# Optimization experiments

Measured on AMD Instinct MI355X. Metric: run time of the kernel, lower is better.

## Reference

```python
import jax, jax.numpy as jnp
import numpy as np

N = 100000          # nodes
E = 3200000         # edges (avg degree 32)
NODE_IN = 128
H = 64              # hidden_feats
B = 2048            # graphs in batch
MP_STEPS = 3
S2S_STEPS = 3
D = 3 * H           # Set2Set in_channels = 192
READOUT = 1024


def setup_inputs() -> dict:
    key = jax.random.key(0)
    ks = jax.random.split(key, 32)
    p = lambda k, shape: (jax.random.normal(k, shape, dtype=jnp.float32) * 0.05)
    inp = {
        "x": jax.random.normal(ks[0], (N, NODE_IN), dtype=jnp.float32),
        "edge_index": jax.random.randint(ks[1], (2, E), 0, N, dtype=jnp.int64),
        "edge_attr": jax.random.normal(ks[2], (E, 16), dtype=jnp.float32),
        "batch": jnp.sort(jax.random.randint(ks[3], (N,), 0, B, dtype=jnp.int64)),
        # project_node_feats
        "W_p": p(ks[4], (H, NODE_IN)), "b_p": p(ks[5], (H,)),
        # SAGEConv: lin_l (on mean-aggregated neighbors, with bias) + lin_r (root, no bias)
        "W_l": p(ks[6], (H, H)), "b_l": p(ks[7], (H,)), "W_r": p(ks[8], (H, H)),
        # gate nets (Linear(H,1)+Sigmoid)
        "gs_W": p(ks[9], (1, H)), "gs_b": p(ks[10], (1,)),
        "gr_W": p(ks[11], (1, H)), "gr_b": p(ks[12], (1,)),
        # GRU_s / GRU_r (single layer, gate order r,z,n as in torch)
        "grus_Wih": p(ks[13], (3 * H, H)), "grus_Whh": p(ks[14], (3 * H, H)),
        "grus_bih": p(ks[15], (3 * H,)), "grus_bhh": p(ks[16], (3 * H,)),
        "grur_Wih": p(ks[17], (3 * H, H)), "grur_Whh": p(ks[18], (3 * H, H)),
        "grur_bih": p(ks[19], (3 * H,)), "grur_bhh": p(ks[20], (3 * H,)),
        # Set2Set LSTM: input 2D -> hidden D (gate order i,f,g,o)
        "lstm_Wih": p(ks[21], (4 * D, 2 * D)), "lstm_Whh": p(ks[22], (4 * D, D)),
        "lstm_bih": p(ks[23], (4 * D,)), "lstm_bhh": p(ks[24], (4 * D,)),
        # sparsify: Linear(2D=6H, readout) + PReLU(scalar, init 0.25)
        "W_sp": p(ks[25], (READOUT, 2 * D)), "b_sp": p(ks[26], (READOUT,)),
        "prelu_a": jnp.float32(0.25),
    }
    return inp


def _gru_cell(x, h, Wih, Whh, bih, bhh):
    gi = x @ Wih.T + bih
    gh = h @ Whh.T + bhh
    ir, iz, inn = jnp.split(gi, 3, axis=-1)
    hr, hz, hn = jnp.split(gh, 3, axis=-1)
    r = jax.nn.sigmoid(ir + hr)
    z = jax.nn.sigmoid(iz + hz)
    n = jnp.tanh(inn + r * hn)
    return (1.0 - z) * n + z * h


def _lstm_cell(x, h, c, Wih, Whh, bih, bhh):
    g = x @ Wih.T + bih + h @ Whh.T + bhh
    i, f, gg, o = jnp.split(g, 4, axis=-1)
    c_new = jax.nn.sigmoid(f) * c + jax.nn.sigmoid(i) * jnp.tanh(gg)
    h_new = jax.nn.sigmoid(o) * jnp.tanh(c_new)
    return h_new, c_new


def reference(x, edge_index, edge_attr, batch,
              W_p, b_p, W_l, b_l, W_r, gs_W, gs_b, gr_W, gr_b,
              grus_Wih, grus_Whh, grus_bih, grus_bhh,
              grur_Wih, grur_Whh, grur_bih, grur_bhh,
              lstm_Wih, lstm_Whh, lstm_bih, lstm_bhh,
              W_sp, b_sp, prelu_a):
    src, dst = edge_index[0], edge_index[1]
    deg = jnp.maximum(jax.ops.segment_sum(jnp.ones((E,), x.dtype), dst, num_segments=N), 1.0)

    proj = jax.nn.relu(x @ W_p.T + b_p)                     # [N, H]
    h_s = proj
    h_r = proj
    gates_r = []
    for _ in range(MP_STEPS):
        # SAGEConv(mean): lin_l(mean_j x_j) + lin_r(x_i)
        agg = jax.ops.segment_sum(h_s[src], dst, num_segments=N) / deg[:, None]
        m = agg @ W_l.T + b_l + h_s @ W_r.T
        am = jax.nn.relu(m)
        gate_s = jax.nn.sigmoid(h_s @ gs_W.T + gs_b)        # [N, 1]
        h_s_new = _gru_cell(gate_s * am, h_s, grus_Wih, grus_Whh, grus_bih, grus_bhh)
        gate_r = jax.nn.sigmoid(h_r @ gr_W.T + gr_b)        # [N, 1]
        gates_r.append(gate_r)
        h_r = _gru_cell(gate_r * am, h_r, grur_Wih, grur_Whh, grur_bih, grur_bhh)
        h_s = h_s_new

    feats = jnp.concatenate([proj, h_s, h_r], axis=1)       # [N, 3H=D]

    # Set2Set readout over ragged graph segments
    q_star = jnp.zeros((B, 2 * D), feats.dtype)
    hl = jnp.zeros((B, D), feats.dtype)
    cl = jnp.zeros((B, D), feats.dtype)
    for _ in range(S2S_STEPS):
        hl, cl = _lstm_cell(q_star, hl, cl, lstm_Wih, lstm_Whh, lstm_bih, lstm_bhh)
        q = hl                                              # [B, D]
        e = jnp.sum(feats * q[batch], axis=-1)              # [N]
        mmax = jax.ops.segment_max(e, batch, num_segments=B)
        ex = jnp.exp(e - mmax[batch])
        denom = jax.ops.segment_sum(ex, batch, num_segments=B)
        a = ex / denom[batch]                               # segment softmax
        r = jax.ops.segment_sum(a[:, None] * feats, batch, num_segments=B)  # [B, D]
        q_star = jnp.concatenate([q, r], axis=1)            # [B, 2D]

    z = q_star @ W_sp.T + b_sp                              # [B, READOUT]
    graph_feats = jnp.where(z >= 0, z, prelu_a * z)         # PReLU
    return graph_feats, jnp.stack(gates_r)                  # [B,1024], [MP_STEPS,N,1]
```

## Files before the change

kernel.cpp:

```cpp
#include <hip/hip_runtime.h>
#include <math.h>

#define NN 100000
#define NE 3200000
#define NIN 128
#define HH 64
#define NB 2048
#define RO 1024

#define NT    1563
#define NBK   391
#define BINB  782
#define GCB   391
#define PCAP  10240
#define PREPN 63488
#define PREPB 248

typedef unsigned short u16;
typedef __attribute__((ext_vector_type(8))) short short8;
typedef __attribute__((ext_vector_type(4))) float f32x4;

__device__ __forceinline__ float sigmoidf_(float x){ return 1.f/(1.f+expf(-x)); }
__device__ __forceinline__ float dot4_(float4 a, float4 b){ return a.x*b.x + a.y*b.y + a.z*b.z + a.w*b.w; }
__device__ __forceinline__ u16 f2bf(float f){
  unsigned u = __float_as_uint(f);
  return (u16)((u + 0x7FFFu + ((u>>16)&1u)) >> 16);
}
__device__ __forceinline__ float bf2f(u16 v){
  return __uint_as_float(((unsigned)v) << 16);
}

__global__ void k_bkcnt_prep(const int* __restrict__ dst, const int* __restrict__ batch,
                             int* __restrict__ bkcnt, int* __restrict__ gcnt,
                             const float* __restrict__ Wp, const float* __restrict__ Wl,
                             const float* __restrict__ Wr,
                             const float* __restrict__ sWih, const float* __restrict__ sWhh,
                             const float* __restrict__ rWih, const float* __restrict__ rWhh,
                             const float* __restrict__ lWih, const float* __restrict__ lWhh,
                             u16* __restrict__ pB_proj, u16* __restrict__ pB_sage,
                             u16* __restrict__ pB_gruS, u16* __restrict__ pB_gruR,
                             u16* __restrict__ pB_lstm){
  __shared__ int hist[NBK];
  const int t = threadIdx.x;
  if (blockIdx.x < BINB){
    for (int i = t; i < NBK; i += 256) hist[i] = 0;
    __syncthreads();
    const int e0 = blockIdx.x * 4096;
    const int cntE = min(4096, NE - e0);
    for (int idx = t; idx < cntE; idx += 256)
      atomicAdd(&hist[dst[e0 + idx] >> 8], 1);
    __syncthreads();
    for (int i = t; i < NBK; i += 256)
      if (hist[i]) atomicAdd(&bkcnt[i], hist[i]);
    return;
  }
  int r = blockIdx.x - BINB;
  if (r < GCB){
    int n = r*256 + t;
    if (n < NN) atomicAdd(&gcnt[batch[n]], 1);
    return;
  }
  int id = (r - GCB)*256 + t;
  if (id >= PREPN) return;
  const float* sp; u16* d;
  if (id < 1024){
    int fi = id; d = pB_proj + (size_t)fi*8;
    int lane = fi&63, kt=(fi>>6)&3, ct=fi>>8;
    int rr = ct*16 + (lane&15), k0 = kt*32 + (lane>>4)*8;
    sp = &Wp[(size_t)rr*NIN + k0];
  } else if (id < 2048){
    int fi = id - 1024; d = pB_sage + (size_t)fi*8;
    int lane = fi&63, kt=(fi>>6)&3, ct=fi>>8;
    int rr = ct*16 + (lane&15), k0 = kt*32 + (lane>>4)*8;
    sp = (k0 < 64) ? &Wl[(size_t)rr*HH + k0] : &Wr[(size_t)rr*HH + (k0-64)];
  } else if (id < 8192){
    int base = id - 2048;
    const float* Wih; const float* Whh; u16* pb; int fi;
    if (base < 3072){ pb = pB_gruS; Wih = sWih; Whh = sWhh; fi = base; }
    else            { pb = pB_gruR; Wih = rWih; Whh = rWhh; fi = base - 3072; }
    int lane = fi&63, kt=(fi>>6)&1, c2=fi>>7;
    const float* W2 = (c2 < 12) ? Wih : Whh;
    int ct = (c2 < 12) ? c2 : c2 - 12;
    int rr = ct*16 + (lane&15), k0 = kt*32 + (lane>>4)*8;
    sp = &W2[(size_t)rr*HH + k0];
    d = pb + (size_t)fi*8;
  } else {
    int fi = id - 8192;
    int ctg = fi / 1152;
    int rem = fi - ctg*1152;
    int ktg = rem >> 6, lane = rem & 63;
    int rr = ctg*16 + (lane&15), k0 = ktg*32 + (lane>>4)*8;
    sp = (k0 < 384) ? &lWih[(size_t)rr*384 + k0] : &lWhh[(size_t)rr*192 + (k0-384)];
    d = pB_lstm + (size_t)fi*8;
  }
  #pragma unroll
  for (int q = 0; q < 8; ++q) d[q] = f2bf(sp[q]);
}

__global__ __launch_bounds__(256) void k_scan_small(
    const int* __restrict__ bkcnt, int* __restrict__ bkbase, int* __restrict__ bcur,
    const int* __restrict__ gcnt, int* __restrict__ growptr){
  __shared__ int sb[256];
  const int t = threadIdx.x;
  if (blockIdx.x == 0){
    int loc[2]; int s = 0;
    #pragma unroll
    for (int q = 0; q < 2; ++q){ int i = t*2+q; loc[q] = (i < NBK) ? bkcnt[i] : 0; s += loc[q]; }
    sb[t] = s; __syncthreads();
    int v = s;
    for (int o = 1; o < 256; o <<= 1){
      int u = (t >= o) ? sb[t-o] : 0; __syncthreads();
      sb[t] += u; __syncthreads();
    }
    int run = sb[t] - v;
    #pragma unroll
    for (int q = 0; q < 2; ++q){
      int i = t*2+q;
      if (i < NBK){ bkbase[i] = run; bcur[i] = run; run += loc[q]; }
    }
    if (t == 255) bkbase[NBK] = run;
  } else {
    int base = t*8;
    int loc[8]; int s = 0;
    #pragma unroll
    for (int q = 0; q < 8; ++q){ loc[q] = gcnt[base+q]; s += loc[q]; }
    sb[t] = s; __syncthreads();
    int v = s;
    for (int o = 1; o < 256; o <<= 1){
      int u = (t >= o) ? sb[t-o] : 0; __syncthreads();
      sb[t] += u; __syncthreads();
    }
    int run = sb[t] - v;
    #pragma unroll
    for (int q = 0; q < 8; ++q){ growptr[base+q] = run; run += loc[q]; }
    if (t == 255) growptr[NB] = run;
  }
}

__global__ __launch_bounds__(256) void k_bin(
    const int* __restrict__ src, const int* __restrict__ dst,
    int* __restrict__ bcur, int2* __restrict__ binned)
{
  __shared__ int hist[NBK];
  __shared__ int lbase[NBK];
  __shared__ int gbase[NBK];
  __shared__ int sb[512];
  __shared__ int2 stage[4096];
  const int t = threadIdx.x;
  const int e0 = blockIdx.x * 4096;
  const int cntE = min(4096, NE - e0);
  for (int i = t; i < NBK; i += 256) hist[i] = 0;
  __syncthreads();
  int2 ed[16];
  #pragma unroll
  for (int k = 0; k < 16; ++k){
    int idx = (k<<8) + t;
    if (idx < cntE){
      int e = e0 + idx;
      ed[k].x = src[e]; ed[k].y = dst[e];
      atomicAdd(&hist[ed[k].y >> 8], 1);
    } else ed[k].y = -1;
  }
  __syncthreads();
  sb[t]     = (t < NBK) ? hist[t] : 0;
  sb[t+256] = (t+256 < NBK) ? hist[t+256] : 0;
  __syncthreads();
  for (int off = 1; off < 512; off <<= 1){
    int v0 = (t >= off)     ? sb[t-off]     : 0;
    int v1 = (t+256 >= off) ? sb[t+256-off] : 0;
    __syncthreads();
    sb[t] += v0; sb[t+256] += v1;
    __syncthreads();
  }
  if (t < NBK)     lbase[t]     = sb[t]     - hist[t];
  if (t+256 < NBK) lbase[t+256] = sb[t+256] - hist[t+256];
  if (t < NBK)     gbase[t]     = (hist[t]     > 0) ? atomicAdd(&bcur[t],     hist[t])     : 0;
  if (t+256 < NBK) gbase[t+256] = (hist[t+256] > 0) ? atomicAdd(&bcur[t+256], hist[t+256]) : 0;
  __syncthreads();
  for (int i = t; i < NBK; i += 256) hist[i] = 0;
  __syncthreads();
  #pragma unroll
  for (int k = 0; k < 16; ++k){
    if (ed[k].y >= 0){
      int b = ed[k].y >> 8;
      int r = atomicAdd(&hist[b], 1);
      stage[lbase[b] + r] = ed[k];
    }
  }
  __syncthreads();
  for (int i = t; i < cntE; i += 256){
    int2 e = stage[i];
    int b = e.y >> 8;
    binned[gbase[b] + (i - lbase[b])] = e;
  }
}

__global__ __launch_bounds__(256) void k_place(
    const int2* __restrict__ binned, const int* __restrict__ bkbase,
    int* __restrict__ rowptr, int* __restrict__ col)
{
  __shared__ int h[256];
  __shared__ int cur[256];
  __shared__ int sb2[256];
  __shared__ int stage[PCAP];
  const int t = threadIdx.x;
  const int b = blockIdx.x;
  const int n0 = b << 8;
  const int B0 = bkbase[b], B1 = bkbase[b+1];
  const int cntE = B1 - B0;
  h[t] = 0; __syncthreads();
  for (int i = t; i < cntE; i += 256){
    int2 e = binned[B0 + i];
    atomicAdd(&h[e.y - n0], 1);
  }
  __syncthreads();
  sb2[t] = h[t]; __syncthreads();
  for (int off = 1; off < 256; off <<= 1){
    int v = (t >= off) ? sb2[t-off] : 0;
    __syncthreads();
    sb2[t] += v;
    __syncthreads();
  }
  int pre = sb2[t] - h[t];
  if (n0 + t < NN) rowptr[n0 + t] = B0 + pre;
  if (b == NBK-1 && t == 0) rowptr[NN] = B1;
  if (cntE <= PCAP){
    cur[t] = pre;
    __syncthreads();
    for (int i = t; i < cntE; i += 256){
      int2 e = binned[B0 + i];
      int idx = atomicAdd(&cur[e.y - n0], 1);
      stage[idx] = e.x;
    }
    __syncthreads();
    for (int i = t; i < cntE; i += 256) col[B0 + i] = stage[i];
  } else {
    cur[t] = B0 + pre;
    __syncthreads();
    for (int i = t; i < cntE; i += 256){
      int2 e = binned[B0 + i];
      int p = atomicAdd(&cur[e.y - n0], 1);
      col[p] = e.x;
    }
  }
}

__global__ __launch_bounds__(256) void k_proj(
    const float* __restrict__ x, const u16* __restrict__ pB, const float* __restrict__ bp,
    float* __restrict__ proj, float* __restrict__ hs, float* __restrict__ hr,
    u16* __restrict__ hsb)
{
  __shared__ u16 s_a[64][136];
  __shared__ u16 s_b[4*4*64*8];
  __shared__ float s_bias[64];
  const int t = threadIdx.x;
  const int n0 = blockIdx.x * 64;
  for (int idx = t; idx < 1024; idx += 256)
    ((short8*)s_b)[idx] = ((const short8*)pB)[idx];
  if (t < 64) s_bias[t] = bp[t];
  {
    int r = t>>2, cg = t&3, node = n0 + r;
    u16* d = &s_a[r][cg*32];
    if (node < NN){
      const float4* xp = (const float4*)&x[(size_t)node*NIN + cg*32];
      #pragma unroll
      for (int q = 0; q < 8; ++q){
        float4 v = xp[q];
        d[q*4+0]=f2bf(v.x); d[q*4+1]=f2bf(v.y); d[q*4+2]=f2bf(v.z); d[q*4+3]=f2bf(v.w);
      }
    } else {
      #pragma unroll
      for (int q = 0; q < 32; ++q) d[q] = 0;
    }
  }
  __syncthreads();
  const int lane = t & 63, nt = t >> 6;
  const int colp = lane & 15, rowg = lane >> 4;
  f32x4 acc[4];
  #pragma unroll
  for (int i = 0; i < 4; ++i) acc[i] = (f32x4){0.f,0.f,0.f,0.f};
  #pragma unroll
  for (int kt = 0; kt < 4; ++kt){
    short8 a = *(const short8*)&s_a[nt*16 + colp][kt*32 + rowg*8];
    #pragma unroll
    for (int ct = 0; ct < 4; ++ct){
      short8 b = *(const short8*)&s_b[((ct*4 + kt)*64 + lane)*8];
      acc[ct] = __builtin_amdgcn_mfma_f32_16x16x32_bf16(a, b, acc[ct], 0, 0, 0);
    }
  }
  #pragma unroll
  for (int reg = 0; reg < 4; ++reg){
    int node = n0 + nt*16 + rowg*4 + reg;
    if (node >= NN) continue;
    #pragma unroll
    for (int ct = 0; ct < 4; ++ct){
      int j = ct*16 + colp;
      float v = fmaxf(acc[ct][reg] + s_bias[j], 0.f);
      size_t o = (size_t)node*HH + j;
      proj[o] = v; hs[o] = v; hr[o] = v;
      hsb[o] = f2bf(v);
    }
  }
}

__global__ __launch_bounds__(256) void k_agg(
    const u16* __restrict__ hb, const int* __restrict__ rowptr,
    const int* __restrict__ col, u16* __restrict__ aggb)
{
  int node = blockIdx.x*4 + (threadIdx.x >> 6);
  int lane = threadIdx.x & 63;
  if (node >= NN) return;
  int beg = rowptr[node], end = rowptr[node+1];
  const int slot = lane >> 3;
  const int c8 = (lane & 7) * 8;
  float a0=0.f,a1=0.f,a2=0.f,a3=0.f,a4=0.f,a5=0.f,a6=0.f,a7=0.f;
  for (int i = beg + slot; i < end; i += 8){
    int nb = col[i];
    short8 v = *(const short8*)&hb[(size_t)nb*HH + c8];
    a0 += bf2f((u16)v[0]); a1 += bf2f((u16)v[1]);
    a2 += bf2f((u16)v[2]); a3 += bf2f((u16)v[3]);
    a4 += bf2f((u16)v[4]); a5 += bf2f((u16)v[5]);
    a6 += bf2f((u16)v[6]); a7 += bf2f((u16)v[7]);
  }
  #pragma unroll
  for (int m = 8; m <= 32; m <<= 1){
    a0 += __shfl_xor(a0, m); a1 += __shfl_xor(a1, m);
    a2 += __shfl_xor(a2, m); a3 += __shfl_xor(a3, m);
    a4 += __shfl_xor(a4, m); a5 += __shfl_xor(a5, m);
    a6 += __shfl_xor(a6, m); a7 += __shfl_xor(a7, m);
  }
  if (slot == 0){
    float invd = 1.f / fmaxf((float)(end - beg), 1.f);
    short8 o;
    o[0]=(short)f2bf(a0*invd); o[1]=(short)f2bf(a1*invd);
    o[2]=(short)f2bf(a2*invd); o[3]=(short)f2bf(a3*invd);
    o[4]=(short)f2bf(a4*invd); o[5]=(short)f2bf(a5*invd);
    o[6]=(short)f2bf(a6*invd); o[7]=(short)f2bf(a7*invd);
    *(short8*)&aggb[(size_t)node*HH + c8] = o;
  }
}

__global__ __launch_bounds__(256) void k_sage(
    const u16* __restrict__ hsb, const u16* __restrict__ pB,
    const float* __restrict__ bl, u16* __restrict__ aggb)
{
  __shared__ u16 s_a[64][136];
  __shared__ u16 s_b[4*4*64*8];
  __shared__ float s_bias[64];
  const int t = threadIdx.x;
  const int n0 = blockIdx.x * 64;
  for (int idx = t; idx < 1024; idx += 256)
    ((short8*)s_b)[idx] = ((const short8*)pB)[idx];
  if (t < 64) s_bias[t] = bl[t];
  {
    int r = t>>2, cg = t&3, node = n0 + r;
    short8* d8 = (short8*)&s_a[r][cg*32];
    if (node < NN){
      const short8* sp = (cg < 2) ? (const short8*)&aggb[(size_t)node*HH + cg*32]
                                  : (const short8*)&hsb[(size_t)node*HH + (cg-2)*32];
      d8[0] = sp[0]; d8[1] = sp[1]; d8[2] = sp[2]; d8[3] = sp[3];
    } else {
      u16* dz = (u16*)d8;
      #pragma unroll
      for (int q = 0; q < 32; ++q) dz[q] = 0;
    }
  }
  __syncthreads();
  const int lane = t & 63, nt = t >> 6;
  const int colp = lane & 15, rowg = lane >> 4;
  f32x4 acc[4];
  #pragma unroll
  for (int i = 0; i < 4; ++i) acc[i] = (f32x4){0.f,0.f,0.f,0.f};
  #pragma unroll
  for (int kt = 0; kt < 4; ++kt){
    short8 a = *(const short8*)&s_a[nt*16 + colp][kt*32 + rowg*8];
    #pragma unroll
    for (int ct = 0; ct < 4; ++ct){
      short8 b = *(const short8*)&s_b[((ct*4 + kt)*64 + lane)*8];
      acc[ct] = __builtin_amdgcn_mfma_f32_16x16x32_bf16(a, b, acc[ct], 0, 0, 0);
    }
  }
  __syncthreads();
  #pragma unroll
  for (int reg = 0; reg < 4; ++reg){
    int node = n0 + nt*16 + rowg*4 + reg;
    if (node >= NN) continue;
    #pragma unroll
    for (int ct = 0; ct < 4; ++ct){
      int j = ct*16 + colp;
      float v = fmaxf(acc[ct][reg] + s_bias[j], 0.f);
      aggb[(size_t)node*HH + j] = f2bf(v);
    }
  }
}

__global__ __launch_bounds__(256) void k_gru(
    float* __restrict__ h, const u16* __restrict__ amb,
    const float* __restrict__ gW, const float* __restrict__ gb,
    const u16* __restrict__ pB,
    const float* __restrict__ bih, const float* __restrict__ bhh,
    float* __restrict__ out_gate, u16* __restrict__ bfout)
{
  __shared__ u16 s_b[2*12*2*64*8];
  __shared__ u16 s_x[64][72];
  __shared__ u16 s_h[64][72];
  __shared__ float s_bi[192], s_bh[192];
  const int t = threadIdx.x;
  const int n0 = blockIdx.x * 64;
  for (int idx = t; idx < 3072; idx += 256)
    ((short8*)s_b)[idx] = ((const short8*)pB)[idx];
  if (t < 192){ s_bi[t] = bih[t]; s_bh[t] = bhh[t]; }
  const float gb0 = gb[0];
  {
    int r = t>>2, cg = t&3, node = n0 + r;
    u16* dh = &s_h[r][cg*16];
    u16* dx = &s_x[r][cg*16];
    if (node < NN){
      float hv[16];
      const float4* hp = (const float4*)&h[(size_t)node*HH + cg*16];
      #pragma unroll
      for (int q = 0; q < 4; ++q){
        float4 v = hp[q];
        hv[q*4+0]=v.x; hv[q*4+1]=v.y; hv[q*4+2]=v.z; hv[q*4+3]=v.w;
      }
      const float* gwp = &gW[cg*16];
      float p = 0.f;
      #pragma unroll
      for (int q = 0; q < 16; ++q) p += hv[q]*gwp[q];
      p += __shfl_xor(p, 1);
      p += __shfl_xor(p, 2);
      float gate = sigmoidf_(p + gb0);
      if (out_gate != nullptr && cg == 0) out_gate[node] = gate;
      #pragma unroll
      for (int q = 0; q < 16; ++q) dh[q] = f2bf(hv[q]);
      const short8* ap = (const short8*)&amb[(size_t)node*HH + cg*16];
      short8 a0 = ap[0], a1 = ap[1];
      #pragma unroll
      for (int q = 0; q < 8; ++q){
        dx[q]   = f2bf(gate * bf2f((u16)a0[q]));
        dx[8+q] = f2bf(gate * bf2f((u16)a1[q]));
      }
    } else {
      #pragma unroll
      for (int q = 0; q < 16; ++q){ dh[q] = 0; dx[q] = 0; }
    }
  }
  __syncthreads();
  const int lane = t & 63, nt = t >> 6;
  const int colp = lane & 15, rowg = lane >> 4;
  f32x4 acc[24];
  #pragma unroll
  for (int i = 0; i < 24; ++i) acc[i] = (f32x4){0.f,0.f,0.f,0.f};
  const int arow = nt*16 + colp;
  #pragma unroll
  for (int kt = 0; kt < 2; ++kt){
    short8 ax = *(const short8*)&s_x[arow][kt*32 + rowg*8];
    short8 ah = *(const short8*)&s_h[arow][kt*32 + rowg*8];
    #pragma unroll
    for (int ct = 0; ct < 12; ++ct){
      short8 b0 = *(const short8*)&s_b[((ct*2 + kt)*64 + lane)*8];
      acc[ct] = __builtin_amdgcn_mfma_f32_16x16x32_bf16(ax, b0, acc[ct], 0, 0, 0);
      short8 b1 = *(const short8*)&s_b[(((12 + ct)*2 + kt)*64 + lane)*8];
      acc[12+ct] = __builtin_amdgcn_mfma_f32_16x16x32_bf16(ah, b1, acc[12+ct], 0, 0, 0);
    }
  }
  #pragma unroll
  for (int reg = 0; reg < 4; ++reg){
    int node = n0 + nt*16 + rowg*4 + reg;
    if (node >= NN) continue;
    #pragma unroll
    for (int jt = 0; jt < 4; ++jt){
      int j = jt*16 + colp;
      float ir = acc[jt][reg]      + s_bi[j];
      float iz = acc[4+jt][reg]    + s_bi[64+j];
      float in_ = acc[8+jt][reg]   + s_bi[128+j];
      float hr_ = acc[12+jt][reg]  + s_bh[j];
      float hz = acc[16+jt][reg]   + s_bh[64+j];
      float hn = acc[20+jt][reg]   + s_bh[128+j];
      float rg = sigmoidf_(ir + hr_);
      float zg = sigmoidf_(iz + hz);
      float ng = tanhf(in_ + rg*hn);
      size_t o = (size_t)node*HH + j;
      float ho = h[o];
      float hv = (1.f - zg)*ng + zg*ho;
      h[o] = hv;
      if (bfout != nullptr) bfout[o] = f2bf(hv);
    }
  }
}

__global__ __launch_bounds__(256) void k_lstmg(
    const float* __restrict__ q_star, const float* __restrict__ hin,
    const u16* __restrict__ pBl, const float* __restrict__ bih, const float* __restrict__ bhh,
    float* __restrict__ gbuf)
{
  __shared__ u16 s_a[64][72];
  __shared__ u16 s_b[6*2*64*8];
  const int t = threadIdx.x;
  const int mt = blockIdx.x >> 3, ntile = blockIdx.x & 7;
  const int g0 = mt * 64, c0 = ntile * 96;
  const int lane = t & 63, nt = t >> 6;
  const int colp = lane & 15, rowg = lane >> 4;
  f32x4 acc[6];
  #pragma unroll
  for (int ct = 0; ct < 6; ++ct){
    int j = c0 + ct*16 + colp;
    float bb = bih[j] + bhh[j];
    acc[ct] = (f32x4){bb, bb, bb, bb};
  }
  const int r = t>>2, cg = t&3;
  for (int kc = 0; kc < 9; ++kc){
    {
      const float* srcp = (kc < 6) ? &q_star[(size_t)(g0+r)*384 + kc*64 + cg*16]
                                   : &hin[(size_t)(g0+r)*192 + (kc-6)*64 + cg*16];
      u16* d = &s_a[r][cg*16];
      const float4* xp = (const float4*)srcp;
      #pragma unroll
      for (int q = 0; q < 4; ++q){
        float4 v = xp[q];
        d[q*4+0]=f2bf(v.x); d[q*4+1]=f2bf(v.y); d[q*4+2]=f2bf(v.z); d[q*4+3]=f2bf(v.w);
      }
    }
    for (int idx2 = t; idx2 < 768; idx2 += 256){
      int ctl = idx2 >> 7, rem = idx2 & 127;
      int ktl = rem >> 6, lane2 = rem & 63;
      int fsrc = ((ntile*6 + ctl)*18 + (kc*2 + ktl))*64 + lane2;
      ((short8*)s_b)[(ctl*2 + ktl)*64 + lane2] = ((const short8*)pBl)[fsrc];
    }
    __syncthreads();
    const int arow = nt*16 + colp;
    #pragma unroll
    for (int ktl = 0; ktl < 2; ++ktl){
      short8 a = *(const short8*)&s_a[arow][ktl*32 + rowg*8];
      #pragma unroll
      for (int ct = 0; ct < 6; ++ct){
        short8 b = *(const short8*)&s_b[((ct*2 + ktl)*64 + lane)*8];
        acc[ct] = __builtin_amdgcn_mfma_f32_16x16x32_bf16(a, b, acc[ct], 0, 0, 0);
      }
    }
    __syncthreads();
  }
  #pragma unroll
  for (int reg = 0; reg < 4; ++reg){
    int g = g0 + nt*16 + rowg*4 + reg;
    #pragma unroll
    for (int ct = 0; ct < 6; ++ct){
      int j = c0 + ct*16 + colp;
      gbuf[(size_t)g*768 + j] = acc[ct][reg];
    }
  }
}

__global__ __launch_bounds__(192) void k_lstm_ep(
    const float* __restrict__ gbuf, const float* __restrict__ cin,
    float* __restrict__ hout, float* __restrict__ cout)
{
  const int g = blockIdx.x, d = threadIdx.x;
  const float* gp = &gbuf[(size_t)g*768];
  float i_ = gp[d], f_ = gp[192+d], gg = gp[384+d], o_ = gp[576+d];
  float c = sigmoidf_(f_)*cin[(size_t)g*192 + d] + sigmoidf_(i_)*tanhf(gg);
  float hn = sigmoidf_(o_)*tanhf(c);
  cout[(size_t)g*192 + d] = c;
  hout[(size_t)g*192 + d] = hn;
}

__global__ __launch_bounds__(256) void k_attn2(
    const float* __restrict__ proj, const float* __restrict__ hs, const float* __restrict__ hr,
    const float* __restrict__ hl, const int* __restrict__ growptr,
    float* __restrict__ q_star)
{
  __shared__ float s_q[192];
  __shared__ float s_e[512];
  __shared__ float red[256];
  const int b = blockIdx.x;
  const int beg = growptr[b], end = growptr[b+1];
  const int cnt = end - beg;
  const int t = threadIdx.x, wv = t>>6, lane = t&63;
  if (t < 192) s_q[t] = hl[(size_t)b*192 + t];
  __syncthreads();
  const float q0 = s_q[lane], q1 = s_q[64+lane], q2 = s_q[128+lane];
  const float* fbase = (t < 64) ? proj : (t < 128) ? hs : hr;
  const int fcol = lane;
  float m_run = -3.0e38f, d_run = 0.f, racc = 0.f;
  for (int c0 = 0; c0 < cnt; c0 += 512){
    int cc = min(512, cnt - c0);
    for (int i = wv; i < cc; i += 4){
      size_t o = (size_t)(beg + c0 + i)*HH;
      float v = proj[o+lane]*q0 + hs[o+lane]*q1 + hr[o+lane]*q2;
      #pragma unroll
      for (int off = 32; off > 0; off >>= 1) v += __shfl_down(v, off);
      if (lane == 0) s_e[i] = v;
    }
    __syncthreads();
    float mx = -3.0e38f;
    for (int i = t; i < cc; i += 256) mx = fmaxf(mx, s_e[i]);
    red[t] = mx; __syncthreads();
    for (int s = 128; s > 0; s >>= 1){ if (t < s) red[t] = fmaxf(red[t], red[t+s]); __syncthreads(); }
    float nm = fmaxf(m_run, red[0]);
    __syncthreads();
    float ps = 0.f;
    for (int i = t; i < cc; i += 256){ float ex = expf(s_e[i] - nm); s_e[i] = ex; ps += ex; }
    red[t] = ps; __syncthreads();
    for (int s = 128; s > 0; s >>= 1){ if (t < s) red[t] += red[t+s]; __syncthreads(); }
    float scale = (m_run > -1.0e38f) ? expf(m_run - nm) : 0.f;
    d_run = d_run*scale + red[0];
    racc *= scale;
    if (t < 192){
      for (int i = 0; i < cc; ++i)
        racc += s_e[i] * fbase[(size_t)(beg + c0 + i)*HH + fcol];
    }
    m_run = nm;
    __syncthreads();
  }
  if (t < 192){
    q_star[(size_t)b*384 + t] = s_q[t];
    q_star[(size_t)b*384 + 192 + t] = (cnt > 0) ? racc/d_run : 0.f;
  }
}

__global__ __launch_bounds__(256) void k_final(
    const float* __restrict__ q_star, const float* __restrict__ W, const float* __restrict__ bias,
    const float* __restrict__ prelu_a, float* __restrict__ out)
{
  __shared__ float s_q[8][384];
  const int t = threadIdx.x;
  const int b0 = blockIdx.x * 8;
  for (int i = t; i < 8*384; i += 256){ int g=i/384, k=i%384; s_q[g][k] = q_star[(size_t)(b0+g)*384 + k]; }
  __syncthreads();
  float a = prelu_a[0];
  float acc[4][8];
  #pragma unroll
  for (int m = 0; m < 4; ++m){
    float bb = bias[t + 256*m];
    #pragma unroll
    for (int g = 0; g < 8; ++g) acc[m][g] = bb;
  }
  for (int k4 = 0; k4 < 96; ++k4){
    float4 w0 = *(const float4*)&W[(size_t)(t)*384     + k4*4];
    float4 w1 = *(const float4*)&W[(size_t)(t+256)*384 + k4*4];
    float4 w2 = *(const float4*)&W[(size_t)(t+512)*384 + k4*4];
    float4 w3 = *(const float4*)&W[(size_t)(t+768)*384 + k4*4];
    #pragma unroll
    for (int g = 0; g < 8; ++g){
      float4 q = *(const float4*)&s_q[g][k4*4];
      acc[0][g] += dot4_(w0,q); acc[1][g] += dot4_(w1,q);
      acc[2][g] += dot4_(w2,q); acc[3][g] += dot4_(w3,q);
    }
  }
  #pragma unroll
  for (int m = 0; m < 4; ++m){
    int j = t + 256*m;
    #pragma unroll
    for (int g = 0; g < 8; ++g){
      float z = acc[m][g];
      out[(size_t)(b0+g)*RO + j] = (z >= 0.f) ? z : a*z;
    }
  }
}

extern "C" void kernel_launch(void* const* d_in, const int* in_sizes, int n_in,
                              void* d_out, int out_size, void* d_ws, size_t ws_size,
                              hipStream_t stream) {
  const float* x       = (const float*)d_in[0];
  const int*   ei      = (const int*)d_in[1];
  const int*   batch   = (const int*)d_in[3];
  const float* W_p     = (const float*)d_in[4];
  const float* b_p     = (const float*)d_in[5];
  const float* W_l     = (const float*)d_in[6];
  const float* b_l     = (const float*)d_in[7];
  const float* W_r     = (const float*)d_in[8];
  const float* gs_W    = (const float*)d_in[9];
  const float* gs_b    = (const float*)d_in[10];
  const float* gr_W    = (const float*)d_in[11];
  const float* gr_b    = (const float*)d_in[12];
  const float* grus_Wih= (const float*)d_in[13];
  const float* grus_Whh= (const float*)d_in[14];
  const float* grus_bih= (const float*)d_in[15];
  const float* grus_bhh= (const float*)d_in[16];
  const float* grur_Wih= (const float*)d_in[17];
  const float* grur_Whh= (const float*)d_in[18];
  const float* grur_bih= (const float*)d_in[19];
  const float* grur_bhh= (const float*)d_in[20];
  const float* lstm_Wih= (const float*)d_in[21];
  const float* lstm_Whh= (const float*)d_in[22];
  const float* lstm_bih= (const float*)d_in[23];
  const float* lstm_bhh= (const float*)d_in[24];
  const float* W_sp    = (const float*)d_in[25];
  const float* b_sp    = (const float*)d_in[26];
  const float* prelu_a = (const float*)d_in[27];

  float* out = (float*)d_out;
  char* w = (char*)d_ws;
  size_t off = 0;
  auto A = [&](size_t bytes){ size_t o = off; off += (bytes + 255) & ~(size_t)255; return o; };

  int*   bkcnt   = (int*)(w + A((size_t)NBK*4));
  int*   bkbase  = (int*)(w + A((size_t)(NBK+1)*4));
  int*   bcur    = (int*)(w + A((size_t)NBK*4));
  int*   rowptr  = (int*)(w + A((size_t)(NN+1)*4));
  int*   col     = (int*)(w + A((size_t)NE*4));
  int2*  binned  = (int2*)(w + A((size_t)NE*8));
  int*   gcnt    = (int*)(w + A((size_t)NB*4));
  int*   growptr = (int*)(w + A((size_t)(NB+1)*4));
  float* proj    = (float*)(w + A((size_t)NN*HH*4));
  float* hs      = (float*)(w + A((size_t)NN*HH*4));
  float* hr      = (float*)(w + A((size_t)NN*HH*4));
  u16*   hsb     = (u16*)(w + A((size_t)NN*HH*2));
  u16*   aggb    = (u16*)(w + A((size_t)NN*HH*2));
  float* qstar   = (float*)(w + A((size_t)NB*384*4));
  float* hlA     = (float*)(w + A((size_t)NB*192*4));
  float* clA     = (float*)(w + A((size_t)NB*192*4));
  float* hlB     = (float*)(w + A((size_t)NB*192*4));
  float* clB     = (float*)(w + A((size_t)NB*192*4));
  float* gbuf    = (float*)(w + A((size_t)NB*768*4));
  u16*   pB_proj = (u16*)(w + A((size_t)8192*2));
  u16*   pB_sage = (u16*)(w + A((size_t)8192*2));
  u16*   pB_gruS = (u16*)(w + A((size_t)24576*2));
  u16*   pB_gruR = (u16*)(w + A((size_t)24576*2));
  u16*   pB_lstm = (u16*)(w + A((size_t)55296*8*2));

  const int* src = ei;
  const int* dst = ei + NE;

  hipMemsetAsync(bkcnt, 0, (size_t)NBK*4, stream);
  hipMemsetAsync(gcnt,  0, (size_t)NB*4, stream);
  hipMemsetAsync(qstar, 0, (size_t)NB*384*4, stream);
  hipMemsetAsync(hlA,   0, (size_t)NB*192*4, stream);
  hipMemsetAsync(clA,   0, (size_t)NB*192*4, stream);

  k_bkcnt_prep<<<BINB + GCB + PREPB, 256, 0, stream>>>(dst, batch, bkcnt, gcnt,
                                                       W_p, W_l, W_r, grus_Wih, grus_Whh,
                                                       grur_Wih, grur_Whh, lstm_Wih, lstm_Whh,
                                                       pB_proj, pB_sage, pB_gruS, pB_gruR, pB_lstm);
  k_scan_small<<<2, 256, 0, stream>>>(bkcnt, bkbase, bcur, gcnt, growptr);
  k_bin  <<<BINB, 256, 0, stream>>>(src, dst, bcur, binned);
  k_place<<<NBK, 256, 0, stream>>>(binned, bkbase, rowptr, col);
  k_proj <<<NT, 256, 0, stream>>>(x, pB_proj, b_p, proj, hs, hr, hsb);

  float* gates_out = out + (size_t)NB*RO;
  for (int s = 0; s < 3; ++s){
    k_agg <<<NN/4, 256, 0, stream>>>(hsb, rowptr, col, aggb);
    k_sage<<<NT, 256, 0, stream>>>(hsb, pB_sage, b_l, aggb);
    k_gru <<<NT, 256, 0, stream>>>(hs, aggb, gs_W, gs_b, pB_gruS,
                                   grus_bih, grus_bhh, (float*)nullptr, hsb);
    k_gru <<<NT, 256, 0, stream>>>(hr, aggb, gr_W, gr_b, pB_gruR,
                                   grur_bih, grur_bhh, gates_out + (size_t)s*NN, (u16*)nullptr);
  }

  float* hin = hlA; float* cin = clA; float* hout = hlB; float* cout_ = clB;
  for (int t = 0; t < 3; ++t){
    k_lstmg  <<<256, 256, 0, stream>>>(qstar, hin, pB_lstm, lstm_bih, lstm_bhh, gbuf);
    k_lstm_ep<<<NB, 192, 0, stream>>>(gbuf, cin, hout, cout_);
    k_attn2  <<<NB, 256, 0, stream>>>(proj, hs, hr, hout, growptr, qstar);
    float* th = hin; hin = hout; hout = th;
    float* tc = cin; cin = cout_; cout_ = tc;
  }

  k_final<<<NB/8, 256, 0, stream>>>(qstar, W_sp, b_sp, prelu_a, out);
}
```

Baseline: 843.3 us.

## Pack binned edges, merge GRU launches, fuse LSTM epilogue, use bf16 feats and MFMA readout

Edges are binned as a single packed int (17-bit src plus 8-bit local dst), which halves binned traffic in k_bin and k_place. The two GRU kernels per step are merged into one launch with twice the blocks. The LSTM epilogue is fused into the attention kernel. Set2Set attention now reads bf16 copies of proj/hs/hr instead of fp32. The final readout linear becomes a bf16 MFMA GEMM with pre-packed weights. The bf16 reads and bf16 GEMM lower precision, and the packing assumes src fits in 17 bits (N=100000 does).

```diff
diff --git a/kernel.cpp b/kernel.cpp
--- a/kernel.cpp
+++ b/kernel.cpp
@@ -13,15 +13,15 @@
 #define BINB  782
 #define GCB   391
 #define PCAP  10240
-#define PREPN 63488
-#define PREPB 248
+#define PREPN 112640
+#define PREPB 440
+#define SRCMASK 0x1FFFF
 
 typedef unsigned short u16;
 typedef __attribute__((ext_vector_type(8))) short short8;
 typedef __attribute__((ext_vector_type(4))) float f32x4;
 
 __device__ __forceinline__ float sigmoidf_(float x){ return 1.f/(1.f+expf(-x)); }
-__device__ __forceinline__ float dot4_(float4 a, float4 b){ return a.x*b.x + a.y*b.y + a.z*b.z + a.w*b.w; }
 __device__ __forceinline__ u16 f2bf(float f){
   unsigned u = __float_as_uint(f);
   return (u16)((u + 0x7FFFu + ((u>>16)&1u)) >> 16);
@@ -37,9 +37,10 @@
                              const float* __restrict__ sWih, const float* __restrict__ sWhh,
                              const float* __restrict__ rWih, const float* __restrict__ rWhh,
                              const float* __restrict__ lWih, const float* __restrict__ lWhh,
+                             const float* __restrict__ Wsp,
                              u16* __restrict__ pB_proj, u16* __restrict__ pB_sage,
                              u16* __restrict__ pB_gruS, u16* __restrict__ pB_gruR,
-                             u16* __restrict__ pB_lstm){
+                             u16* __restrict__ pB_lstm, u16* __restrict__ pB_fin){
   __shared__ int hist[NBK];
   const int t = threadIdx.x;
   if (blockIdx.x < BINB){
@@ -84,7 +85,7 @@
     int rr = ct*16 + (lane&15), k0 = kt*32 + (lane>>4)*8;
     sp = &W2[(size_t)rr*HH + k0];
     d = pb + (size_t)fi*8;
-  } else {
+  } else if (id < 63488){
     int fi = id - 8192;
     int ctg = fi / 1152;
     int rem = fi - ctg*1152;
@@ -92,6 +93,14 @@
     int rr = ctg*16 + (lane&15), k0 = ktg*32 + (lane>>4)*8;
     sp = (k0 < 384) ? &lWih[(size_t)rr*384 + k0] : &lWhh[(size_t)rr*192 + (k0-384)];
     d = pB_lstm + (size_t)fi*8;
+  } else {
+    int fi = id - 63488;
+    int ctg = fi / 768;
+    int rem = fi - ctg*768;
+    int ktg = rem >> 6, lane = rem & 63;
+    int rr = ctg*16 + (lane&15), k0 = ktg*32 + (lane>>4)*8;
+    sp = &Wsp[(size_t)rr*384 + k0];
+    d = pB_fin + (size_t)fi*8;
   }
   #pragma unroll
   for (int q = 0; q < 8; ++q) d[q] = f2bf(sp[q]);
@@ -139,13 +148,14 @@
 
 __global__ __launch_bounds__(256) void k_bin(
     const int* __restrict__ src, const int* __restrict__ dst,
-    int* __restrict__ bcur, int2* __restrict__ binned)
+    int* __restrict__ bcur, int* __restrict__ binned)
 {
   __shared__ int hist[NBK];
   __shared__ int lbase[NBK];
   __shared__ int gbase[NBK];
   __shared__ int sb[512];
-  __shared__ int2 stage[4096];
+  __shared__ int stagep[4096];
+  __shared__ u16 stageb[4096];
   const int t = threadIdx.x;
   const int e0 = blockIdx.x * 4096;
   const int cntE = min(4096, NE - e0);
@@ -184,19 +194,20 @@
     if (ed[k].y >= 0){
       int b = ed[k].y >> 8;
       int r = atomicAdd(&hist[b], 1);
-      stage[lbase[b] + r] = ed[k];
+      int p = lbase[b] + r;
+      stagep[p] = ed[k].x | ((ed[k].y & 255) << 17);
+      stageb[p] = (u16)b;
     }
   }
   __syncthreads();
   for (int i = t; i < cntE; i += 256){
-    int2 e = stage[i];
-    int b = e.y >> 8;
-    binned[gbase[b] + (i - lbase[b])] = e;
+    int b = stageb[i];
+    binned[gbase[b] + (i - lbase[b])] = stagep[i];
   }
 }
 
 __global__ __launch_bounds__(256) void k_place(
-    const int2* __restrict__ binned, const int* __restrict__ bkbase,
+    const int* __restrict__ binned, const int* __restrict__ bkbase,
     int* __restrict__ rowptr, int* __restrict__ col)
 {
   __shared__ int h[256];
@@ -210,8 +221,8 @@
   const int cntE = B1 - B0;
   h[t] = 0; __syncthreads();
   for (int i = t; i < cntE; i += 256){
-    int2 e = binned[B0 + i];
-    atomicAdd(&h[e.y - n0], 1);
+    int e = binned[B0 + i];
+    atomicAdd(&h[e >> 17], 1);
   }
   __syncthreads();
   sb2[t] = h[t]; __syncthreads();
@@ -228,9 +239,9 @@
     cur[t] = pre;
     __syncthreads();
     for (int i = t; i < cntE; i += 256){
-      int2 e = binned[B0 + i];
-      int idx = atomicAdd(&cur[e.y - n0], 1);
-      stage[idx] = e.x;
+      int e = binned[B0 + i];
+      int idx = atomicAdd(&cur[e >> 17], 1);
+      stage[idx] = e & SRCMASK;
     }
     __syncthreads();
     for (int i = t; i < cntE; i += 256) col[B0 + i] = stage[i];
@@ -238,17 +249,17 @@
     cur[t] = B0 + pre;
     __syncthreads();
     for (int i = t; i < cntE; i += 256){
-      int2 e = binned[B0 + i];
-      int p = atomicAdd(&cur[e.y - n0], 1);
-      col[p] = e.x;
+      int e = binned[B0 + i];
+      int p = atomicAdd(&cur[e >> 17], 1);
+      col[p] = e & SRCMASK;
     }
   }
 }
 
 __global__ __launch_bounds__(256) void k_proj(
     const float* __restrict__ x, const u16* __restrict__ pB, const float* __restrict__ bp,
-    float* __restrict__ proj, float* __restrict__ hs, float* __restrict__ hr,
-    u16* __restrict__ hsb)
+    float* __restrict__ hs, float* __restrict__ hr,
+    u16* __restrict__ projb, u16* __restrict__ hsb, u16* __restrict__ hrb)
 {
   __shared__ u16 s_a[64][136];
   __shared__ u16 s_b[4*4*64*8];
@@ -297,8 +308,9 @@
       int j = ct*16 + colp;
       float v = fmaxf(acc[ct][reg] + s_bias[j], 0.f);
       size_t o = (size_t)node*HH + j;
-      proj[o] = v; hs[o] = v; hr[o] = v;
-      hsb[o] = f2bf(v);
+      hs[o] = v; hr[o] = v;
+      u16 bv = f2bf(v);
+      projb[o] = bv; hsb[o] = bv; hrb[o] = bv;
     }
   }
 }
@@ -394,19 +406,29 @@
   }
 }
 
-__global__ __launch_bounds__(256) void k_gru(
-    float* __restrict__ h, const u16* __restrict__ amb,
-    const float* __restrict__ gW, const float* __restrict__ gb,
-    const u16* __restrict__ pB,
-    const float* __restrict__ bih, const float* __restrict__ bhh,
-    float* __restrict__ out_gate, u16* __restrict__ bfout)
+__global__ __launch_bounds__(256) void k_gru2(
+    float* __restrict__ hs, float* __restrict__ hr, const u16* __restrict__ amb,
+    const float* __restrict__ gsW, const float* __restrict__ gsb,
+    const float* __restrict__ grW, const float* __restrict__ grb,
+    const u16* __restrict__ pBS, const u16* __restrict__ pBR,
+    const float* __restrict__ sbih, const float* __restrict__ sbhh,
+    const float* __restrict__ rbih, const float* __restrict__ rbhh,
+    float* __restrict__ out_gate, u16* __restrict__ hsb, u16* __restrict__ hrb)
 {
   __shared__ u16 s_b[2*12*2*64*8];
   __shared__ u16 s_x[64][72];
   __shared__ u16 s_h[64][72];
   __shared__ float s_bi[192], s_bh[192];
   const int t = threadIdx.x;
-  const int n0 = blockIdx.x * 64;
+  const bool isR = blockIdx.x >= NT;
+  const int n0 = (isR ? (blockIdx.x - NT) : blockIdx.x) * 64;
+  float* __restrict__ h = isR ? hr : hs;
+  const u16* __restrict__ pB = isR ? pBR : pBS;
+  const float* __restrict__ gW = isR ? grW : gsW;
+  const float* __restrict__ gb = isR ? grb : gsb;
+  const float* __restrict__ bih = isR ? rbih : sbih;
+  const float* __restrict__ bhh = isR ? rbhh : sbhh;
+  u16* __restrict__ bfout = isR ? hrb : hsb;
   for (int idx = t; idx < 3072; idx += 256)
     ((short8*)s_b)[idx] = ((const short8*)pB)[idx];
   if (t < 192){ s_bi[t] = bih[t]; s_bh[t] = bhh[t]; }
@@ -430,7 +452,7 @@
       p += __shfl_xor(p, 1);
       p += __shfl_xor(p, 2);
       float gate = sigmoidf_(p + gb0);
-      if (out_gate != nullptr && cg == 0) out_gate[node] = gate;
+      if (isR && cg == 0) out_gate[node] = gate;
       #pragma unroll
       for (int q = 0; q < 16; ++q) dh[q] = f2bf(hv[q]);
       const short8* ap = (const short8*)&amb[(size_t)node*HH + cg*16];
@@ -484,7 +506,7 @@
       float ho = h[o];
       float hv = (1.f - zg)*ng + zg*ho;
       h[o] = hv;
-      if (bfout != nullptr) bfout[o] = f2bf(hv);
+      bfout[o] = f2bf(hv);
     }
   }
 }
@@ -551,23 +573,11 @@
   }
 }
 
-__global__ __launch_bounds__(192) void k_lstm_ep(
+__global__ __launch_bounds__(256) void k_attn2(
     const float* __restrict__ gbuf, const float* __restrict__ cin,
-    float* __restrict__ hout, float* __restrict__ cout)
-{
-  const int g = blockIdx.x, d = threadIdx.x;
-  const float* gp = &gbuf[(size_t)g*768];
-  float i_ = gp[d], f_ = gp[192+d], gg = gp[384+d], o_ = gp[576+d];
-  float c = sigmoidf_(f_)*cin[(size_t)g*192 + d] + sigmoidf_(i_)*tanhf(gg);
-  float hn = sigmoidf_(o_)*tanhf(c);
-  cout[(size_t)g*192 + d] = c;
-  hout[(size_t)g*192 + d] = hn;
-}
-
-__global__ __launch_bounds__(256) void k_attn2(
-    const float* __restrict__ proj, const float* __restrict__ hs, const float* __restrict__ hr,
-    const float* __restrict__ hl, const int* __restrict__ growptr,
-    float* __restrict__ q_star)
+    float* __restrict__ hout, float* __restrict__ cout,
+    const u16* __restrict__ projb, const u16* __restrict__ hsb, const u16* __restrict__ hrb,
+    const int* __restrict__ growptr, float* __restrict__ q_star)
 {
   __shared__ float s_q[192];
   __shared__ float s_e[512];
@@ -576,17 +586,25 @@
   const int beg = growptr[b], end = growptr[b+1];
   const int cnt = end - beg;
   const int t = threadIdx.x, wv = t>>6, lane = t&63;
-  if (t < 192) s_q[t] = hl[(size_t)b*192 + t];
+  if (t < 192){
+    const float* gp = &gbuf[(size_t)b*768];
+    float i_ = gp[t], f_ = gp[192+t], gg = gp[384+t], o_ = gp[576+t];
+    float c = sigmoidf_(f_)*cin[(size_t)b*192 + t] + sigmoidf_(i_)*tanhf(gg);
+    float hn = sigmoidf_(o_)*tanhf(c);
+    cout[(size_t)b*192 + t] = c;
+    hout[(size_t)b*192 + t] = hn;
+    s_q[t] = hn;
+  }
   __syncthreads();
   const float q0 = s_q[lane], q1 = s_q[64+lane], q2 = s_q[128+lane];
-  const float* fbase = (t < 64) ? proj : (t < 128) ? hs : hr;
+  const u16* fbase = (t < 64) ? projb : (t < 128) ? hsb : hrb;
   const int fcol = lane;
   float m_run = -3.0e38f, d_run = 0.f, racc = 0.f;
   for (int c0 = 0; c0 < cnt; c0 += 512){
     int cc = min(512, cnt - c0);
     for (int i = wv; i < cc; i += 4){
       size_t o = (size_t)(beg + c0 + i)*HH;
-      float v = proj[o+lane]*q0 + hs[o+lane]*q1 + hr[o+lane]*q2;
+      float v = bf2f(projb[o+lane])*q0 + bf2f(hsb[o+lane])*q1 + bf2f(hrb[o+lane])*q2;
       #pragma unroll
       for (int off = 32; off > 0; off >>= 1) v += __shfl_down(v, off);
       if (lane == 0) s_e[i] = v;
@@ -607,7 +625,7 @@
     racc *= scale;
     if (t < 192){
       for (int i = 0; i < cc; ++i)
-        racc += s_e[i] * fbase[(size_t)(beg + c0 + i)*HH + fcol];
+        racc += s_e[i] * bf2f(fbase[(size_t)(beg + c0 + i)*HH + fcol]);
     }
     m_run = nm;
     __syncthreads();
@@ -618,42 +636,64 @@
   }
 }
 
-__global__ __launch_bounds__(256) void k_final(
-    const float* __restrict__ q_star, const float* __restrict__ W, const float* __restrict__ bias,
-    const float* __restrict__ prelu_a, float* __restrict__ out)
+__global__ __launch_bounds__(256) void k_fing(
+    const float* __restrict__ q_star, const u16* __restrict__ pBf,
+    const float* __restrict__ bias, const float* __restrict__ prelu_a,
+    float* __restrict__ out)
 {
-  __shared__ float s_q[8][384];
+  __shared__ u16 s_a[64][72];
+  __shared__ u16 s_b[8*2*64*8];
   const int t = threadIdx.x;
-  const int b0 = blockIdx.x * 8;
-  for (int i = t; i < 8*384; i += 256){ int g=i/384, k=i%384; s_q[g][k] = q_star[(size_t)(b0+g)*384 + k]; }
-  __syncthreads();
-  float a = prelu_a[0];
-  float acc[4][8];
-  #pragma unroll
-  for (int m = 0; m < 4; ++m){
-    float bb = bias[t + 256*m];
-    #pragma unroll
-    for (int g = 0; g < 8; ++g) acc[m][g] = bb;
-  }
-  for (int k4 = 0; k4 < 96; ++k4){
-    float4 w0 = *(const float4*)&W[(size_t)(t)*384     + k4*4];
-    float4 w1 = *(const float4*)&W[(size_t)(t+256)*384 + k4*4];
-    float4 w2 = *(const float4*)&W[(size_t)(t+512)*384 + k4*4];
-    float4 w3 = *(const float4*)&W[(size_t)(t+768)*384 + k4*4];
-    #pragma unroll
-    for (int g = 0; g < 8; ++g){
-      float4 q = *(const float4*)&s_q[g][k4*4];
-      acc[0][g] += dot4_(w0,q); acc[1][g] += dot4_(w1,q);
-      acc[2][g] += dot4_(w2,q); acc[3][g] += dot4_(w3,q);
-    }
-  }
-  #pragma unroll
-  for (int m = 0; m < 4; ++m){
-    int j = t + 256*m;
-    #pragma unroll
-    for (int g = 0; g < 8; ++g){
-      float z = acc[m][g];
-      out[(size_t)(b0+g)*RO + j] = (z >= 0.f) ? z : a*z;
+  const int mt = blockIdx.x >> 3, ntile = blockIdx.x & 7;
+  const int g0 = mt * 64, c0 = ntile * 128;
+  const int lane = t & 63, nt = t >> 6;
+  const int colp = lane & 15, rowg = lane >> 4;
+  f32x4 acc[8];
+  #pragma unroll
+  for (int ct = 0; ct < 8; ++ct){
+    float bb = bias[c0 + ct*16 + colp];
+    acc[ct] = (f32x4){bb, bb, bb, bb};
+  }
+  const int r = t>>2, cg = t&3;
+  for (int kc = 0; kc < 6; ++kc){
+    {
+      const float* srcp = &q_star[(size_t)(g0+r)*384 + kc*64 + cg*16];
+      u16* d = &s_a[r][cg*16];
+      const float4* xp = (const float4*)srcp;
+      #pragma unroll
+      for (int q = 0; q < 4; ++q){
+        float4 v = xp[q];
+        d[q*4+0]=f2bf(v.x); d[q*4+1]=f2bf(v.y); d[q*4+2]=f2bf(v.z); d[q*4+3]=f2bf(v.w);
+      }
+    }
+    for (int idx2 = t; idx2 < 1024; idx2 += 256){
+      int ctl = idx2 >> 7, rem = idx2 & 127;
+      int ktl = rem >> 6, lane2 = rem & 63;
+      int fsrc = (ntile*8 + ctl)*768 + (kc*2 + ktl)*64 + lane2;
+      ((short8*)s_b)[(ctl*2 + ktl)*64 + lane2] = ((const short8*)pBf)[fsrc];
+    }
+    __syncthreads();
+    const int arow = nt*16 + colp;
+    #pragma unroll
+    for (int ktl = 0; ktl < 2; ++ktl){
+      short8 a = *(const short8*)&s_a[arow][ktl*32 + rowg*8];
+      #pragma unroll
+      for (int ct = 0; ct < 8; ++ct){
+        short8 b = *(const short8*)&s_b[((ct*2 + ktl)*64 + lane)*8];
+        acc[ct] = __builtin_amdgcn_mfma_f32_16x16x32_bf16(a, b, acc[ct], 0, 0, 0);
+      }
+    }
+    __syncthreads();
+  }
+  const float a = prelu_a[0];
+  #pragma unroll
+  for (int reg = 0; reg < 4; ++reg){
+    int g = g0 + nt*16 + rowg*4 + reg;
+    #pragma unroll
+    for (int ct = 0; ct < 8; ++ct){
+      int j = c0 + ct*16 + colp;
+      float z = acc[ct][reg];
+      out[(size_t)g*RO + j] = (z >= 0.f) ? z : a*z;
     }
   }
 }
@@ -699,13 +739,14 @@
   int*   bcur    = (int*)(w + A((size_t)NBK*4));
   int*   rowptr  = (int*)(w + A((size_t)(NN+1)*4));
   int*   col     = (int*)(w + A((size_t)NE*4));
-  int2*  binned  = (int2*)(w + A((size_t)NE*8));
+  int*   binned  = (int*)(w + A((size_t)NE*4));
   int*   gcnt    = (int*)(w + A((size_t)NB*4));
   int*   growptr = (int*)(w + A((size_t)(NB+1)*4));
-  float* proj    = (float*)(w + A((size_t)NN*HH*4));
   float* hs      = (float*)(w + A((size_t)NN*HH*4));
   float* hr      = (float*)(w + A((size_t)NN*HH*4));
+  u16*   projb   = (u16*)(w + A((size_t)NN*HH*2));
   u16*   hsb     = (u16*)(w + A((size_t)NN*HH*2));
+  u16*   hrb     = (u16*)(w + A((size_t)NN*HH*2));
   u16*   aggb    = (u16*)(w + A((size_t)NN*HH*2));
   float* qstar   = (float*)(w + A((size_t)NB*384*4));
   float* hlA     = (float*)(w + A((size_t)NB*192*4));
@@ -718,6 +759,7 @@
   u16*   pB_gruS = (u16*)(w + A((size_t)24576*2));
   u16*   pB_gruR = (u16*)(w + A((size_t)24576*2));
   u16*   pB_lstm = (u16*)(w + A((size_t)55296*8*2));
+  u16*   pB_fin  = (u16*)(w + A((size_t)49152*8*2));
 
   const int* src = ei;
   const int* dst = ei + NE;
@@ -730,31 +772,31 @@
 
   k_bkcnt_prep<<<BINB + GCB + PREPB, 256, 0, stream>>>(dst, batch, bkcnt, gcnt,
                                                        W_p, W_l, W_r, grus_Wih, grus_Whh,
-                                                       grur_Wih, grur_Whh, lstm_Wih, lstm_Whh,
-                                                       pB_proj, pB_sage, pB_gruS, pB_gruR, pB_lstm);
+                                                       grur_Wih, grur_Whh, lstm_Wih, lstm_Whh, W_sp,
+                                                       pB_proj, pB_sage, pB_gruS, pB_gruR,
+                                                       pB_lstm, pB_fin);
   k_scan_small<<<2, 256, 0, stream>>>(bkcnt, bkbase, bcur, gcnt, growptr);
   k_bin  <<<BINB, 256, 0, stream>>>(src, dst, bcur, binned);
   k_place<<<NBK, 256, 0, stream>>>(binned, bkbase, rowptr, col);
-  k_proj <<<NT, 256, 0, stream>>>(x, pB_proj, b_p, proj, hs, hr, hsb);
+  k_proj <<<NT, 256, 0, stream>>>(x, pB_proj, b_p, hs, hr, projb, hsb, hrb);
 
   float* gates_out = out + (size_t)NB*RO;
   for (int s = 0; s < 3; ++s){
     k_agg <<<NN/4, 256, 0, stream>>>(hsb, rowptr, col, aggb);
     k_sage<<<NT, 256, 0, stream>>>(hsb, pB_sage, b_l, aggb);
-    k_gru <<<NT, 256, 0, stream>>>(hs, aggb, gs_W, gs_b, pB_gruS,
-                                   grus_bih, grus_bhh, (float*)nullptr, hsb);
-    k_gru <<<NT, 256, 0, stream>>>(hr, aggb, gr_W, gr_b, pB_gruR,
-                                   grur_bih, grur_bhh, gates_out + (size_t)s*NN, (u16*)nullptr);
+    k_gru2<<<2*NT, 256, 0, stream>>>(hs, hr, aggb, gs_W, gs_b, gr_W, gr_b,
+                                     pB_gruS, pB_gruR,
+                                     grus_bih, grus_bhh, grur_bih, grur_bhh,
+                                     gates_out + (size_t)s*NN, hsb, hrb);
   }
 
   float* hin = hlA; float* cin = clA; float* hout = hlB; float* cout_ = clB;
   for (int t = 0; t < 3; ++t){
-    k_lstmg  <<<256, 256, 0, stream>>>(qstar, hin, pB_lstm, lstm_bih, lstm_bhh, gbuf);
-    k_lstm_ep<<<NB, 192, 0, stream>>>(gbuf, cin, hout, cout_);
-    k_attn2  <<<NB, 256, 0, stream>>>(proj, hs, hr, hout, growptr, qstar);
+    k_lstmg<<<256, 256, 0, stream>>>(qstar, hin, pB_lstm, lstm_bih, lstm_bhh, gbuf);
+    k_attn2<<<NB, 256, 0, stream>>>(gbuf, cin, hout, cout_, projb, hsb, hrb, growptr, qstar);
     float* th = hin; hin = hout; hout = th;
     float* tc = cin; cin = cout_; cout_ = tc;
   }
 
-  k_final<<<NB/8, 256, 0, stream>>>(qstar, W_sp, b_sp, prelu_a, out);
-}
+  k_fing<<<256, 256, 0, stream>>>(qstar, pB_fin, b_sp, prelu_a, out);
+}
```

Result: faster. 684.2 us, median of 2 (-18.9%).
